# Kernel optimization log

Hardware: AMD Instinct MI355X
Metric: run time of the kernel (lower is better)

## Reference

```python
import jax, jax.numpy as jnp
import numpy as np

HIDDEN = 2048
N_HEADS = 32
N_KV_HEADS = 8
HEAD_DIM = HIDDEN // N_HEADS  # 64
GROUPS = N_HEADS // N_KV_HEADS  # 4
ROPE_THETA = 10000.0
B, S = 1, 2048


def setup_inputs() -> dict:
    key = jax.random.key(0)
    ks = jax.random.split(key, 5)
    scale = 1.0 / np.sqrt(HIDDEN)
    return {
        "hidden_states": jax.random.normal(ks[0], (B, S, HIDDEN), dtype=jnp.float32),
        "Wq": jax.random.normal(ks[1], (HIDDEN, N_HEADS * HEAD_DIM), dtype=jnp.float32) * scale,
        "Wk": jax.random.normal(ks[2], (HIDDEN, N_KV_HEADS * HEAD_DIM), dtype=jnp.float32) * scale,
        "Wv": jax.random.normal(ks[3], (HIDDEN, N_KV_HEADS * HEAD_DIM), dtype=jnp.float32) * scale,
        "Wo": jax.random.normal(ks[4], (N_HEADS * HEAD_DIM, HIDDEN), dtype=jnp.float32) * scale,
    }


def _rope_tables(seq_len, dtype):
    # freqs_cos/sin buffers: [seq_len, HEAD_DIM//2]
    inv_freq = 1.0 / (ROPE_THETA ** (jnp.arange(0, HEAD_DIM, 2, dtype=jnp.float32) / HEAD_DIM))
    t = jnp.arange(seq_len, dtype=jnp.float32)
    freqs = jnp.outer(t, inv_freq)
    return jnp.cos(freqs).astype(dtype), jnp.sin(freqs).astype(dtype)


def _apply_rope(x, cos, sin):
    # x: [B, H, S, Dh], interleaved even/odd rotation
    xe = x[..., 0::2]
    xo = x[..., 1::2]
    # cos/sin: [S, Dh/2] -> broadcast over batch & heads
    out_e = xe * cos - xo * sin
    out_o = xe * sin + xo * cos
    return jnp.stack([out_e, out_o], axis=-1).reshape(x.shape)


def reference(hidden_states, Wq, Wk, Wv, Wo):
    bsz, q_len, _ = hidden_states.shape
    dtype = hidden_states.dtype

    q = (hidden_states @ Wq).reshape(bsz, q_len, N_HEADS, HEAD_DIM).transpose(0, 2, 1, 3)
    k = (hidden_states @ Wk).reshape(bsz, q_len, N_KV_HEADS, HEAD_DIM).transpose(0, 2, 1, 3)
    v = (hidden_states @ Wv).reshape(bsz, q_len, N_KV_HEADS, HEAD_DIM).transpose(0, 2, 1, 3)

    cos, sin = _rope_tables(q_len, dtype)
    q = _apply_rope(q, cos, sin)
    k = _apply_rope(k, cos, sin)

    # GQA: repeat_interleave kv heads to match query heads
    k = jnp.repeat(k, GROUPS, axis=1)  # [B, H, S, Dh]
    v = jnp.repeat(v, GROUPS, axis=1)

    # attention_mask=None path: no mask applied (matches module default)
    scores = jnp.einsum("bhqd,bhkd->bhqk", q, k) / jnp.sqrt(jnp.asarray(HEAD_DIM, dtype))
    attn = jax.nn.softmax(scores.astype(jnp.float32), axis=-1).astype(dtype)
    out = jnp.einsum("bhqk,bhkd->bhqd", attn, v)
    out = out.transpose(0, 2, 1, 3).reshape(bsz, q_len, N_HEADS * HEAD_DIM)
    return out @ Wo
```

## Files before the change

kernel.cpp:

```cpp
#include <hip/hip_runtime.h>

typedef __bf16 bf16x8 __attribute__((ext_vector_type(8)));
typedef float f32x4 __attribute__((ext_vector_type(4)));
typedef unsigned short u16x4 __attribute__((ext_vector_type(4)));
typedef unsigned short u16x8 __attribute__((ext_vector_type(8)));
typedef unsigned int u32x4 __attribute__((ext_vector_type(4)));

__device__ __forceinline__ float bf2f(unsigned short h) {
    union { unsigned int u; float f; } v;
    v.u = ((unsigned int)h) << 16;
    return v.f;
}
__device__ __forceinline__ unsigned short f2bf(float f) {
    return __builtin_bit_cast(unsigned short, (__bf16)f);
}
__device__ __forceinline__ void glds16(const unsigned short* g, unsigned short* l) {
    __builtin_amdgcn_global_load_lds((__attribute__((address_space(1))) void*)g,
                                     (__attribute__((address_space(3))) void*)l,
                                     16, 0, 0);
}

#define MFMA16(a, b, c) __builtin_amdgcn_mfma_f32_16x16x32_bf16((a), (b), (c), 0, 0, 0)

__global__ __launch_bounds__(256) void prep1(const float* __restrict__ X,
                                             const float* __restrict__ Wq,
                                             const float* __restrict__ Wk,
                                             const float* __restrict__ Wv,
                                             unsigned short* __restrict__ Xbf,
                                             unsigned short* __restrict__ wqkvT) {
    const int b = blockIdx.x;
    const int tid = threadIdx.x;
    if (b < 4096) {
        const int i = (b * 256 + tid) * 4;
        const float4 v = *(const float4*)(X + i);
        u16x4 o;
        o[0] = f2bf(v.x); o[1] = f2bf(v.y); o[2] = f2bf(v.z); o[3] = f2bf(v.w);
        *(u16x4*)(Xbf + i) = o;
        return;
    }
    __shared__ __align__(16) unsigned short tile[32][33];
    const int tx = tid & 31, ty = tid >> 5;
    const int b2 = b - 4096;
    const int kb = (b2 & 63) * 32;
    const int nb = (b2 >> 6) * 32;
    const float* src; int scol, sld;
    if (nb < 2048)      { src = Wq; scol = nb;        sld = 2048; }
    else if (nb < 2560) { src = Wk; scol = nb - 2048; sld = 512;  }
    else                { src = Wv; scol = nb - 2560; sld = 512;  }
#pragma unroll
    for (int i = 0; i < 32; i += 8)
        tile[ty + i][tx] = f2bf(src[(size_t)(kb + ty + i) * sld + (scol + tx)]);
    __syncthreads();
#pragma unroll
    for (int i = 0; i < 32; i += 8)
        wqkvT[(size_t)(nb + ty + i) * 2048 + (kb + tx)] = tile[tx][ty + i];
}

__global__ __launch_bounds__(256) void prep2(const float* __restrict__ Wo,
                                             const unsigned short* __restrict__ qkv,
                                             unsigned short* __restrict__ woT,
                                             unsigned short* __restrict__ vt) {
    const int b = blockIdx.x;
    const int tid = threadIdx.x;
    const int tx = tid & 31, ty = tid >> 5;
    __shared__ __align__(16) unsigned short tile[32][33];
    if (b < 4096) {
        const int kb = (b & 63) * 32;
        const int nb = (b >> 6) * 32;
#pragma unroll
        for (int i = 0; i < 32; i += 8)
            tile[ty + i][tx] = f2bf(Wo[(size_t)(kb + ty + i) * 2048 + (nb + tx)]);
        __syncthreads();
#pragma unroll
        for (int i = 0; i < 32; i += 8)
            woT[(size_t)(nb + ty + i) * 2048 + (kb + tx)] = tile[tx][ty + i];
    } else {
        const int b2 = b - 4096;
        const int bx = (b2 & 15) * 32;
        const int by = (b2 >> 4) * 32;
#pragma unroll
        for (int i = 0; i < 32; i += 8)
            tile[ty + i][tx] = qkv[(size_t)(by + ty + i) * 3072 + 2560 + bx + tx];
        __syncthreads();
#pragma unroll
        for (int i = 0; i < 32; i += 8)
            vt[(size_t)(bx + ty + i) * 2048 + (by + tx)] = tile[tx][ty + i];
    }
}

template <int BM, bool ROPE>
__global__ __launch_bounds__(256) void gemm_bt(const unsigned short* __restrict__ A,
                                               const unsigned short* __restrict__ BT,
                                               void* __restrict__ Cv,
                                               int K, int lda, int ldb, int ldc,
                                               int out_f32) {
    constexpr int MT = BM / 32;
    constexpr int ACALLS = BM / 16;
    __shared__ __align__(16) unsigned short As[BM * 128];
    __shared__ __align__(16) unsigned short Bs[128 * 128];

    const int tid = threadIdx.x;
    const int lane = tid & 63;
    const int wave = tid >> 6;
    const int quad = lane >> 4;
    const int l15 = lane & 15;
    const int bm = blockIdx.x * BM;
    const int bn = blockIdx.y * 128;
    const int wm = (wave & 1) * (BM / 2);
    const int wn = (wave >> 1) * 64;

    const int srow = wave * 4 + (lane >> 4);
    const int sw = (lane & 15) ^ (srow & 7);
    const unsigned short* Ag = A + (size_t)(bm + srow) * lda + sw * 8;
    const unsigned short* Bg = BT + (size_t)(bn + srow) * ldb + sw * 8;
    unsigned short* Asl = As + wave * 512;
    unsigned short* Bsl = Bs + wave * 512;

    f32x4 acc[MT][4] = {};

    for (int k0 = 0; k0 < K; k0 += 128) {
#pragma unroll
        for (int i = 0; i < ACALLS; i++)
            glds16(Ag + (size_t)(16 * i) * lda + k0, Asl + i * 2048);
#pragma unroll
        for (int i = 0; i < 8; i++)
            glds16(Bg + (size_t)(16 * i) * ldb + k0, Bsl + i * 2048);
        __syncthreads();
#pragma unroll
        for (int ks = 0; ks < 4; ks++) {
            bf16x8 af[MT], bfr[4];
#pragma unroll
            for (int mt = 0; mt < MT; mt++) {
                const int row = wm + 16 * mt + l15;
                af[mt] = __builtin_bit_cast(bf16x8,
                    *(const u32x4*)&As[row * 128 + (((quad + 4 * ks) ^ (row & 7)) * 8)]);
            }
#pragma unroll
            for (int nt = 0; nt < 4; nt++) {
                const int row = wn + 16 * nt + l15;
                bfr[nt] = __builtin_bit_cast(bf16x8,
                    *(const u32x4*)&Bs[row * 128 + (((quad + 4 * ks) ^ (row & 7)) * 8)]);
            }
#pragma unroll
            for (int mt = 0; mt < MT; mt++)
#pragma unroll
                for (int nt = 0; nt < 4; nt++)
                    acc[mt][nt] = MFMA16(af[mt], bfr[nt], acc[mt][nt]);
        }
        __syncthreads();
    }

    if (ROPE) {
#pragma unroll
        for (int mt = 0; mt < MT; mt++) {
#pragma unroll
            for (int nt = 0; nt < 4; nt++) {
                const int col = bn + wn + 16 * nt + l15;
                if (col < 2560) {
                    const int i = (col & 63) >> 1;
                    const float inv = exp2f(-0.41524101186092036f * (float)i);
                    const float sign = (col & 1) ? 1.0f : -1.0f;
#pragma unroll
                    for (int r = 0; r < 4; r++) {
                        const int row = bm + wm + 16 * mt + quad * 4 + r;
                        float sn, cs;
                        __sincosf((float)row * inv, &sn, &cs);
                        const float partner = __shfl_xor(acc[mt][nt][r], 1, 64);
                        acc[mt][nt][r] = acc[mt][nt][r] * cs + sign * partner * sn;
                    }
                }
            }
        }
    }

#pragma unroll
    for (int mt = 0; mt < MT; mt++) {
#pragma unroll
        for (int nt = 0; nt < 4; nt++) {
#pragma unroll
            for (int r = 0; r < 4; r++) {
                const int row = bm + wm + 16 * mt + quad * 4 + r;
                const int col = bn + wn + 16 * nt + l15;
                if (out_f32)
                    ((float*)Cv)[(size_t)row * ldc + col] = acc[mt][nt][r];
                else
                    ((unsigned short*)Cv)[(size_t)row * ldc + col] = f2bf(acc[mt][nt][r]);
            }
        }
    }
}

__global__ __launch_bounds__(256) void attn_kernel(const unsigned short* __restrict__ qkv,
                                                   const unsigned short* __restrict__ vt,
                                                   unsigned short* __restrict__ attn_out) {
    const int qb = blockIdx.x;
    const int h = blockIdx.y;
    const int kvh = h >> 2;
    const int tid = threadIdx.x;
    const int lane = tid & 63;
    const int wave = tid >> 6;
    const int quad = lane >> 4;
    const int l15 = lane & 15;
    const int w0 = qb * 128 + wave * 32;

    __shared__ __align__(16) unsigned short Ks[128 * 64];
    __shared__ __align__(16) unsigned short Vs[64 * 128];
    __shared__ __align__(16) unsigned short St[4][32][72];
    unsigned short (*Sw)[72] = St[wave];

    const int srow = wave * 8 + (lane >> 3);
    const int swK = (lane & 7) ^ (srow & 7);
    const unsigned short* Kg = qkv + 2048 + kvh * 64 + swK * 8;
    unsigned short* Ksl = Ks + wave * 512;
    const int vrow = wave * 4 + (lane >> 4);
    const int swV = (lane & 15) ^ (vrow & 7);
    const unsigned short* Vg = vt + (size_t)(kvh * 64 + vrow) * 2048 + swV * 8;
    unsigned short* Vsl = Vs + wave * 512;

    bf16x8 qf[2][2];
#pragma unroll
    for (int mt = 0; mt < 2; mt++)
#pragma unroll
        for (int ks = 0; ks < 2; ks++) {
            u32x4 raw = *(const u32x4*)&qkv[(size_t)(w0 + 16 * mt + l15) * 3072 + h * 64 + quad * 8 + 32 * ks];
            u16x8 t = __builtin_bit_cast(u16x8, raw);
#pragma unroll
            for (int j = 0; j < 8; j++) t[j] = f2bf(bf2f(t[j]) * 0.125f);
            qf[mt][ks] = __builtin_bit_cast(bf16x8, t);
        }

    bf16x8 ones;
#pragma unroll
    for (int j = 0; j < 8; j++) ones[j] = (__bf16)1.0f;

    f32x4 acc_o[2][4] = {};
    f32x4 acc_l[2] = {};

    const float LOG2E = 1.44269504088896f;
    const float MB = -17.3123404906676f;

    for (int kb2 = 0; kb2 < 16; kb2++) {
        const int kbase = kb2 * 128;
#pragma unroll
        for (int i = 0; i < 4; i++) {
            glds16(Kg + (size_t)(kbase + srow + 32 * i) * 3072, Ksl + i * 2048);
            glds16(Vg + (size_t)(16 * i) * 2048 + kbase, Vsl + i * 2048);
        }
        __syncthreads();

#pragma unroll
        for (int kh = 0; kh < 2; kh++) {
            f32x4 st[2][4] = {};
#pragma unroll
            for (int n = 0; n < 4; n++) {
                const int row = kh * 64 + 16 * n + l15;
                const bf16x8 kf0 = __builtin_bit_cast(bf16x8,
                    *(const u32x4*)&Ks[row * 64 + ((quad ^ (l15 & 7)) * 8)]);
                const bf16x8 kf1 = __builtin_bit_cast(bf16x8,
                    *(const u32x4*)&Ks[row * 64 + (((quad + 4) ^ (l15 & 7)) * 8)]);
#pragma unroll
                for (int mt = 0; mt < 2; mt++) {
                    st[mt][n] = MFMA16(kf0, qf[mt][0], st[mt][n]);
                    st[mt][n] = MFMA16(kf1, qf[mt][1], st[mt][n]);
                }
            }

#pragma unroll
            for (int mt = 0; mt < 2; mt++)
#pragma unroll
                for (int n = 0; n < 4; n++) {
                    u16x4 pk;
#pragma unroll
                    for (int r = 0; r < 4; r++)
                        pk[r] = f2bf(exp2f(fmaf(st[mt][n][r], LOG2E, MB)));
                    *(u16x4*)&Sw[16 * mt + l15][16 * n + quad * 4] = pk;
                }

            bf16x8 pf[2][2];
#pragma unroll
            for (int mt = 0; mt < 2; mt++) {
                pf[mt][0] = __builtin_bit_cast(bf16x8, *(const u32x4*)&Sw[16 * mt + l15][quad * 8]);
                pf[mt][1] = __builtin_bit_cast(bf16x8, *(const u32x4*)&Sw[16 * mt + l15][quad * 8 + 32]);
            }

#pragma unroll
            for (int mt = 0; mt < 2; mt++) {
                acc_l[mt] = MFMA16(pf[mt][0], ones, acc_l[mt]);
                acc_l[mt] = MFMA16(pf[mt][1], ones, acc_l[mt]);
            }

#pragma unroll
            for (int nt = 0; nt < 4; nt++) {
                const int row = 16 * nt + l15;
                const int c0 = kh * 8 + (quad ^ (l15 & 7));
                const int c1 = kh * 8 + ((quad + 4) ^ (l15 & 7));
                const bf16x8 vf0 = __builtin_bit_cast(bf16x8, *(const u32x4*)&Vs[row * 128 + c0 * 8]);
                const bf16x8 vf1 = __builtin_bit_cast(bf16x8, *(const u32x4*)&Vs[row * 128 + c1 * 8]);
#pragma unroll
                for (int mt = 0; mt < 2; mt++) {
                    acc_o[mt][nt] = MFMA16(pf[mt][0], vf0, acc_o[mt][nt]);
                    acc_o[mt][nt] = MFMA16(pf[mt][1], vf1, acc_o[mt][nt]);
                }
            }
        }
        __syncthreads();
    }

#pragma unroll
    for (int mt = 0; mt < 2; mt++) {
        float linv[4];
#pragma unroll
        for (int r = 0; r < 4; r++) linv[r] = 1.0f / acc_l[mt][r];
#pragma unroll
        for (int nt = 0; nt < 4; nt++)
#pragma unroll
            for (int r = 0; r < 4; r++)
                attn_out[(size_t)(w0 + 16 * mt + quad * 4 + r) * 2048 + h * 64 + 16 * nt + l15] =
                    f2bf(acc_o[mt][nt][r] * linv[r]);
    }
}

extern "C" void kernel_launch(void* const* d_in, const int* in_sizes, int n_in,
                              void* d_out, int out_size, void* d_ws, size_t ws_size,
                              hipStream_t stream) {
    (void)in_sizes; (void)n_in; (void)out_size; (void)ws_size;

    const float* X  = (const float*)d_in[0];
    const float* Wq = (const float*)d_in[1];
    const float* Wk = (const float*)d_in[2];
    const float* Wv = (const float*)d_in[3];
    const float* Wo = (const float*)d_in[4];

    unsigned short* ws16  = (unsigned short*)d_ws;
    unsigned short* Xbf   = ws16;
    unsigned short* wqkvT = ws16 + (size_t)4194304;
    unsigned short* qkv   = (unsigned short*)d_out;
    unsigned short* vt    = ws16;
    unsigned short* attnO = ws16 + (size_t)1048576;
    unsigned short* woT   = ws16 + (size_t)5242880;

    prep1<<<10240, 256, 0, stream>>>(X, Wq, Wk, Wv, Xbf, wqkvT);

    gemm_bt<64, true><<<dim3(32, 24), 256, 0, stream>>>(Xbf, wqkvT, qkv, 2048, 2048, 2048, 3072, 0);

    prep2<<<5120, 256, 0, stream>>>(Wo, qkv, woT, vt);

    attn_kernel<<<dim3(16, 32), 256, 0, stream>>>(qkv, vt, attnO);

    gemm_bt<64, false><<<dim3(32, 16), 256, 0, stream>>>(attnO, woT, (void*)d_out, 2048, 2048, 2048, 2048, 1);
}
```

Before: 244.5 us.

## Double-buffer K/V tiles in attention to overlap loads with compute

Measured after the change: 237.6 us. -2.8%, faster.

```diff
diff --git a/kernel.cpp b/kernel.cpp
--- a/kernel.cpp
+++ b/kernel.cpp
@@ -201,21 +201,20 @@
     const int wave = tid >> 6;
     const int quad = lane >> 4;
     const int l15 = lane & 15;
+    const int l7 = l15 & 7;
     const int w0 = qb * 128 + wave * 32;
 
-    __shared__ __align__(16) unsigned short Ks[128 * 64];
-    __shared__ __align__(16) unsigned short Vs[64 * 128];
+    __shared__ __align__(16) unsigned short Ks[2][64 * 64];
+    __shared__ __align__(16) unsigned short Vs[2][64 * 64];
     __shared__ __align__(16) unsigned short St[4][32][72];
     unsigned short (*Sw)[72] = St[wave];
 
     const int srow = wave * 8 + (lane >> 3);
-    const int swK = (lane & 7) ^ (srow & 7);
-    const unsigned short* Kg = qkv + 2048 + kvh * 64 + swK * 8;
-    unsigned short* Ksl = Ks + wave * 512;
-    const int vrow = wave * 4 + (lane >> 4);
-    const int swV = (lane & 15) ^ (vrow & 7);
-    const unsigned short* Vg = vt + (size_t)(kvh * 64 + vrow) * 2048 + swV * 8;
-    unsigned short* Vsl = Vs + wave * 512;
+    const int sw8 = (lane & 7) ^ (srow & 7);
+    const unsigned short* Kg = qkv + 2048 + kvh * 64 + sw8 * 8;
+    const unsigned short* Vg = vt + (size_t)(kvh * 64 + srow) * 2048 + sw8 * 8;
+    unsigned short* Ksl = &Ks[0][wave * 512];
+    unsigned short* Vsl = &Vs[0][wave * 512];
 
     bf16x8 qf[2][2];
 #pragma unroll
@@ -239,72 +238,85 @@
     const float LOG2E = 1.44269504088896f;
     const float MB = -17.3123404906676f;
 
-    for (int kb2 = 0; kb2 < 16; kb2++) {
-        const int kbase = kb2 * 128;
-#pragma unroll
-        for (int i = 0; i < 4; i++) {
-            glds16(Kg + (size_t)(kbase + srow + 32 * i) * 3072, Ksl + i * 2048);
-            glds16(Vg + (size_t)(16 * i) * 2048 + kbase, Vsl + i * 2048);
-        }
-        __syncthreads();
-
-#pragma unroll
-        for (int kh = 0; kh < 2; kh++) {
-            f32x4 st[2][4] = {};
+#define STAGE_KV(kt, b) do {                                             \
+        const size_t kb_ = (size_t)(kt) * 64;                            \
+        glds16(Kg + (kb_ + srow) * 3072,      Ksl + (b) * 4096);         \
+        glds16(Kg + (kb_ + srow + 32) * 3072, Ksl + (b) * 4096 + 2048);  \
+        glds16(Vg + kb_,                      Vsl + (b) * 4096);         \
+        glds16(Vg + 32 * 2048 + kb_,          Vsl + (b) * 4096 + 2048);  \
+    } while (0)
+
+    STAGE_KV(0, 0);
+
+    for (int kt = 0; kt < 32; kt++) {
+        const int cur = kt & 1;
+        if (kt < 31) {
+            STAGE_KV(kt + 1, cur ^ 1);
+            asm volatile("s_waitcnt vmcnt(4)" ::: "memory");
+        } else {
+            asm volatile("s_waitcnt vmcnt(0)" ::: "memory");
+        }
+        __builtin_amdgcn_s_barrier();
+
+        const unsigned short* Kb = Ks[cur];
+        const unsigned short* Vb = Vs[cur];
+
+        f32x4 st[2][4] = {};
+#pragma unroll
+        for (int n = 0; n < 4; n++) {
+            const int row = 16 * n + l15;
+            const bf16x8 kf0 = __builtin_bit_cast(bf16x8,
+                *(const u32x4*)&Kb[row * 64 + ((quad ^ l7) * 8)]);
+            const bf16x8 kf1 = __builtin_bit_cast(bf16x8,
+                *(const u32x4*)&Kb[row * 64 + (((quad + 4) ^ l7) * 8)]);
+#pragma unroll
+            for (int mt = 0; mt < 2; mt++) {
+                st[mt][n] = MFMA16(kf0, qf[mt][0], st[mt][n]);
+                st[mt][n] = MFMA16(kf1, qf[mt][1], st[mt][n]);
+            }
+        }
+
+#pragma unroll
+        for (int mt = 0; mt < 2; mt++)
 #pragma unroll
             for (int n = 0; n < 4; n++) {
-                const int row = kh * 64 + 16 * n + l15;
-                const bf16x8 kf0 = __builtin_bit_cast(bf16x8,
-                    *(const u32x4*)&Ks[row * 64 + ((quad ^ (l15 & 7)) * 8)]);
-                const bf16x8 kf1 = __builtin_bit_cast(bf16x8,
-                    *(const u32x4*)&Ks[row * 64 + (((quad + 4) ^ (l15 & 7)) * 8)]);
-#pragma unroll
-                for (int mt = 0; mt < 2; mt++) {
-                    st[mt][n] = MFMA16(kf0, qf[mt][0], st[mt][n]);
-                    st[mt][n] = MFMA16(kf1, qf[mt][1], st[mt][n]);
-                }
-            }
-
-#pragma unroll
-            for (int mt = 0; mt < 2; mt++)
-#pragma unroll
-                for (int n = 0; n < 4; n++) {
-                    u16x4 pk;
-#pragma unroll
-                    for (int r = 0; r < 4; r++)
-                        pk[r] = f2bf(exp2f(fmaf(st[mt][n][r], LOG2E, MB)));
-                    *(u16x4*)&Sw[16 * mt + l15][16 * n + quad * 4] = pk;
-                }
-
-            bf16x8 pf[2][2];
+                u16x4 pk;
+#pragma unroll
+                for (int r = 0; r < 4; r++)
+                    pk[r] = f2bf(exp2f(fmaf(st[mt][n][r], LOG2E, MB)));
+                *(u16x4*)&Sw[16 * mt + l15][16 * n + quad * 4] = pk;
+            }
+
+        bf16x8 pf[2][2];
+#pragma unroll
+        for (int mt = 0; mt < 2; mt++) {
+            pf[mt][0] = __builtin_bit_cast(bf16x8, *(const u32x4*)&Sw[16 * mt + l15][quad * 8]);
+            pf[mt][1] = __builtin_bit_cast(bf16x8, *(const u32x4*)&Sw[16 * mt + l15][quad * 8 + 32]);
+        }
+
+#pragma unroll
+        for (int mt = 0; mt < 2; mt++) {
+            acc_l[mt] = MFMA16(pf[mt][0], ones, acc_l[mt]);
+            acc_l[mt] = MFMA16(pf[mt][1], ones, acc_l[mt]);
+        }
+
+#pragma unroll
+        for (int nt = 0; nt < 4; nt++) {
+            const int row = 16 * nt + l15;
+            const bf16x8 vf0 = __builtin_bit_cast(bf16x8,
+                *(const u32x4*)&Vb[row * 64 + ((quad ^ l7) * 8)]);
+            const bf16x8 vf1 = __builtin_bit_cast(bf16x8,
+                *(const u32x4*)&Vb[row * 64 + (((quad + 4) ^ l7) * 8)]);
 #pragma unroll
             for (int mt = 0; mt < 2; mt++) {
-                pf[mt][0] = __builtin_bit_cast(bf16x8, *(const u32x4*)&Sw[16 * mt + l15][quad * 8]);
-                pf[mt][1] = __builtin_bit_cast(bf16x8, *(const u32x4*)&Sw[16 * mt + l15][quad * 8 + 32]);
-            }
-
-#pragma unroll
-            for (int mt = 0; mt < 2; mt++) {
-                acc_l[mt] = MFMA16(pf[mt][0], ones, acc_l[mt]);
-                acc_l[mt] = MFMA16(pf[mt][1], ones, acc_l[mt]);
-            }
-
-#pragma unroll
-            for (int nt = 0; nt < 4; nt++) {
-                const int row = 16 * nt + l15;
-                const int c0 = kh * 8 + (quad ^ (l15 & 7));
-                const int c1 = kh * 8 + ((quad + 4) ^ (l15 & 7));
-                const bf16x8 vf0 = __builtin_bit_cast(bf16x8, *(const u32x4*)&Vs[row * 128 + c0 * 8]);
-                const bf16x8 vf1 = __builtin_bit_cast(bf16x8, *(const u32x4*)&Vs[row * 128 + c1 * 8]);
-#pragma unroll
-                for (int mt = 0; mt < 2; mt++) {
-                    acc_o[mt][nt] = MFMA16(pf[mt][0], vf0, acc_o[mt][nt]);
-                    acc_o[mt][nt] = MFMA16(pf[mt][1], vf1, acc_o[mt][nt]);
-                }
-            }
-        }
-        __syncthreads();
-    }
+                acc_o[mt][nt] = MFMA16(pf[mt][0], vf0, acc_o[mt][nt]);
+                acc_o[mt][nt] = MFMA16(pf[mt][1], vf1, acc_o[mt][nt]);
+            }
+        }
+
+        __builtin_amdgcn_s_barrier();
+    }
+#undef STAGE_KV
 
 #pragma unroll
     for (int mt = 0; mt < 2; mt++) {
```

## Halve attention query tile per block to double grid and swizzle P scratch

Applied to the files above, without the earlier changes.

New measurement: 239.3 us. 2.1% less time.

```diff
diff --git a/kernel.cpp b/kernel.cpp
--- a/kernel.cpp
+++ b/kernel.cpp
@@ -201,12 +201,13 @@
     const int wave = tid >> 6;
     const int quad = lane >> 4;
     const int l15 = lane & 15;
-    const int w0 = qb * 128 + wave * 32;
+    const int l7 = l15 & 7;
+    const int w0 = qb * 64 + wave * 16;
 
     __shared__ __align__(16) unsigned short Ks[128 * 64];
     __shared__ __align__(16) unsigned short Vs[64 * 128];
-    __shared__ __align__(16) unsigned short St[4][32][72];
-    unsigned short (*Sw)[72] = St[wave];
+    __shared__ __align__(16) unsigned short St[4][16][64];
+    unsigned short (*Sw)[64] = St[wave];
 
     const int srow = wave * 8 + (lane >> 3);
     const int swK = (lane & 7) ^ (srow & 7);
@@ -217,24 +218,22 @@
     const unsigned short* Vg = vt + (size_t)(kvh * 64 + vrow) * 2048 + swV * 8;
     unsigned short* Vsl = Vs + wave * 512;
 
-    bf16x8 qf[2][2];
-#pragma unroll
-    for (int mt = 0; mt < 2; mt++)
-#pragma unroll
-        for (int ks = 0; ks < 2; ks++) {
-            u32x4 raw = *(const u32x4*)&qkv[(size_t)(w0 + 16 * mt + l15) * 3072 + h * 64 + quad * 8 + 32 * ks];
-            u16x8 t = __builtin_bit_cast(u16x8, raw);
-#pragma unroll
-            for (int j = 0; j < 8; j++) t[j] = f2bf(bf2f(t[j]) * 0.125f);
-            qf[mt][ks] = __builtin_bit_cast(bf16x8, t);
-        }
+    bf16x8 qf[2];
+#pragma unroll
+    for (int ks = 0; ks < 2; ks++) {
+        u32x4 raw = *(const u32x4*)&qkv[(size_t)(w0 + l15) * 3072 + h * 64 + quad * 8 + 32 * ks];
+        u16x8 t = __builtin_bit_cast(u16x8, raw);
+#pragma unroll
+        for (int j = 0; j < 8; j++) t[j] = f2bf(bf2f(t[j]) * 0.125f);
+        qf[ks] = __builtin_bit_cast(bf16x8, t);
+    }
 
     bf16x8 ones;
 #pragma unroll
     for (int j = 0; j < 8; j++) ones[j] = (__bf16)1.0f;
 
-    f32x4 acc_o[2][4] = {};
-    f32x4 acc_l[2] = {};
+    f32x4 acc_o[4] = {};
+    f32x4 acc_l = {};
 
     const float LOG2E = 1.44269504088896f;
     const float MB = -17.3123404906676f;
@@ -250,74 +249,59 @@
 
 #pragma unroll
         for (int kh = 0; kh < 2; kh++) {
-            f32x4 st[2][4] = {};
+            f32x4 st[4] = {};
 #pragma unroll
             for (int n = 0; n < 4; n++) {
                 const int row = kh * 64 + 16 * n + l15;
                 const bf16x8 kf0 = __builtin_bit_cast(bf16x8,
-                    *(const u32x4*)&Ks[row * 64 + ((quad ^ (l15 & 7)) * 8)]);
+                    *(const u32x4*)&Ks[row * 64 + ((quad ^ l7) * 8)]);
                 const bf16x8 kf1 = __builtin_bit_cast(bf16x8,
-                    *(const u32x4*)&Ks[row * 64 + (((quad + 4) ^ (l15 & 7)) * 8)]);
-#pragma unroll
-                for (int mt = 0; mt < 2; mt++) {
-                    st[mt][n] = MFMA16(kf0, qf[mt][0], st[mt][n]);
-                    st[mt][n] = MFMA16(kf1, qf[mt][1], st[mt][n]);
-                }
-            }
-
-#pragma unroll
-            for (int mt = 0; mt < 2; mt++)
-#pragma unroll
-                for (int n = 0; n < 4; n++) {
-                    u16x4 pk;
-#pragma unroll
-                    for (int r = 0; r < 4; r++)
-                        pk[r] = f2bf(exp2f(fmaf(st[mt][n][r], LOG2E, MB)));
-                    *(u16x4*)&Sw[16 * mt + l15][16 * n + quad * 4] = pk;
-                }
-
-            bf16x8 pf[2][2];
-#pragma unroll
-            for (int mt = 0; mt < 2; mt++) {
-                pf[mt][0] = __builtin_bit_cast(bf16x8, *(const u32x4*)&Sw[16 * mt + l15][quad * 8]);
-                pf[mt][1] = __builtin_bit_cast(bf16x8, *(const u32x4*)&Sw[16 * mt + l15][quad * 8 + 32]);
-            }
-
-#pragma unroll
-            for (int mt = 0; mt < 2; mt++) {
-                acc_l[mt] = MFMA16(pf[mt][0], ones, acc_l[mt]);
-                acc_l[mt] = MFMA16(pf[mt][1], ones, acc_l[mt]);
-            }
+                    *(const u32x4*)&Ks[row * 64 + (((quad + 4) ^ l7) * 8)]);
+                st[n] = MFMA16(kf0, qf[0], st[n]);
+                st[n] = MFMA16(kf1, qf[1], st[n]);
+            }
+
+            const int gq = quad >> 1, oq = (quad & 1) * 4;
+#pragma unroll
+            for (int n = 0; n < 4; n++) {
+                u16x4 pk;
+#pragma unroll
+                for (int r = 0; r < 4; r++)
+                    pk[r] = f2bf(exp2f(fmaf(st[n][r], LOG2E, MB)));
+                *(u16x4*)&Sw[l15][(((2 * n + gq) ^ l7) << 3) + oq] = pk;
+            }
+
+            const bf16x8 pf0 = __builtin_bit_cast(bf16x8,
+                *(const u32x4*)&Sw[l15][(quad ^ l7) << 3]);
+            const bf16x8 pf1 = __builtin_bit_cast(bf16x8,
+                *(const u32x4*)&Sw[l15][((quad + 4) ^ l7) << 3]);
+
+            acc_l = MFMA16(pf0, ones, acc_l);
+            acc_l = MFMA16(pf1, ones, acc_l);
 
 #pragma unroll
             for (int nt = 0; nt < 4; nt++) {
                 const int row = 16 * nt + l15;
-                const int c0 = kh * 8 + (quad ^ (l15 & 7));
-                const int c1 = kh * 8 + ((quad + 4) ^ (l15 & 7));
+                const int c0 = kh * 8 + (quad ^ l7);
+                const int c1 = kh * 8 + ((quad + 4) ^ l7);
                 const bf16x8 vf0 = __builtin_bit_cast(bf16x8, *(const u32x4*)&Vs[row * 128 + c0 * 8]);
                 const bf16x8 vf1 = __builtin_bit_cast(bf16x8, *(const u32x4*)&Vs[row * 128 + c1 * 8]);
-#pragma unroll
-                for (int mt = 0; mt < 2; mt++) {
-                    acc_o[mt][nt] = MFMA16(pf[mt][0], vf0, acc_o[mt][nt]);
-                    acc_o[mt][nt] = MFMA16(pf[mt][1], vf1, acc_o[mt][nt]);
-                }
-            }
-        }
-        __syncthreads();
-    }
-
-#pragma unroll
-    for (int mt = 0; mt < 2; mt++) {
-        float linv[4];
-#pragma unroll
-        for (int r = 0; r < 4; r++) linv[r] = 1.0f / acc_l[mt][r];
-#pragma unroll
-        for (int nt = 0; nt < 4; nt++)
-#pragma unroll
-            for (int r = 0; r < 4; r++)
-                attn_out[(size_t)(w0 + 16 * mt + quad * 4 + r) * 2048 + h * 64 + 16 * nt + l15] =
-                    f2bf(acc_o[mt][nt][r] * linv[r]);
-    }
+                acc_o[nt] = MFMA16(pf0, vf0, acc_o[nt]);
+                acc_o[nt] = MFMA16(pf1, vf1, acc_o[nt]);
+            }
+        }
+        __syncthreads();
+    }
+
+    float linv[4];
+#pragma unroll
+    for (int r = 0; r < 4; r++) linv[r] = 1.0f / acc_l[r];
+#pragma unroll
+    for (int nt = 0; nt < 4; nt++)
+#pragma unroll
+        for (int r = 0; r < 4; r++)
+            attn_out[(size_t)(w0 + quad * 4 + r) * 2048 + h * 64 + 16 * nt + l15] =
+                f2bf(acc_o[nt][r] * linv[r]);
 }
 
 extern "C" void kernel_launch(void* const* d_in, const int* in_sizes, int n_in,
@@ -345,7 +329,7 @@
 
     prep2<<<5120, 256, 0, stream>>>(Wo, qkv, woT, vt);
 
-    attn_kernel<<<dim3(16, 32), 256, 0, stream>>>(qkv, vt, attnO);
+    attn_kernel<<<dim3(32, 32), 256, 0, stream>>>(qkv, vt, attnO);
 
     gemm_bt<64, false><<<dim3(32, 16), 256, 0, stream>>>(attnO, woT, (void*)d_out, 2048, 2048, 2048, 2048, 1);
 }
```
